# Kernel tuning notes

Measured on AMD Instinct MI355X. Metric: run time of the kernel, lower is better.

The kernel has to match this reference:

```python
import jax, jax.numpy as jnp
import numpy as np

B, T, D, H = 8, 1024, 512, 8
D4 = 4 * D
SIGMA = 16.0
EPS = 1e-5


def layer_norm(x, w, b):
    m = jnp.mean(x, axis=-1, keepdims=True)
    v = jnp.mean((x - m) ** 2, axis=-1, keepdims=True)
    return (x - m) * jax.lax.rsqrt(v + EPS) * w + b


def setup_inputs() -> dict:
    key = jax.random.key(0)
    ks = jax.random.split(key, 12)
    return {
        "x": jax.random.normal(ks[0], (B, T, D), jnp.float32),
        "posv": jax.random.randint(ks[1], (B, T), 0, 64, jnp.int32),
        "posh": jax.random.randint(ks[2], (B, T), 0, 64, jnp.int32),
        "norm1_w": jnp.ones((D,), jnp.float32),
        "norm1_b": jnp.zeros((D,), jnp.float32),
        "in_w": jax.random.normal(ks[3], (3 * D, D), jnp.float32) * (D ** -0.5),
        "in_b": jnp.zeros((3 * D,), jnp.float32),
        "out_w": jax.random.normal(ks[4], (D, D), jnp.float32) * (D ** -0.5),
        "out_b": jnp.zeros((D,), jnp.float32),
        "norm2_w": jnp.ones((D,), jnp.float32),
        "norm2_b": jnp.zeros((D,), jnp.float32),
        "w1": jax.random.normal(ks[5], (D4, D), jnp.float32) * (D ** -0.5),
        "b1": jnp.zeros((D4,), jnp.float32),
        "w2": jax.random.normal(ks[6], (D, D4), jnp.float32) * (D4 ** -0.5),
        "b2": jnp.zeros((D,), jnp.float32),
        "gate": jnp.array(0.0, jnp.float32),
    }


def reference(x, posv, posh, norm1_w, norm1_b, in_w, in_b, out_w, out_b,
              norm2_w, norm2_b, w1, b1, w2, b2, gate):
    hd = D // H
    residual = x
    xn = layer_norm(x, norm1_w, norm1_b)

    # --- standard multi-head self-attention (dropout=eval identity) ---
    qkv = xn @ in_w.T + in_b                       # [B,T,3D]
    q, k, v = jnp.split(qkv, 3, axis=-1)
    q = q.reshape(B, T, H, hd).transpose(0, 2, 1, 3)  # [B,H,T,hd]
    k = k.reshape(B, T, H, hd).transpose(0, 2, 1, 3)
    v = v.reshape(B, T, H, hd).transpose(0, 2, 1, 3)
    scores = jnp.einsum("bhqd,bhkd->bhqk", q, k) * (hd ** -0.5)
    attn = jax.nn.softmax(scores, axis=-1)
    ctx = jnp.einsum("bhqk,bhkd->bhqd", attn, v)   # [B,H,T,hd]
    ctx = ctx.transpose(0, 2, 1, 3).reshape(B, T, D)
    std_out = ctx @ out_w.T + out_b

    # --- Gaussian kernel position attention ---
    pos = jnp.stack([posv, posh], axis=-1).astype(jnp.float32)  # [B,T,2]
    dist_sq = jnp.sum((pos[:, :, None, :] - pos[:, None, :, :]) ** 2, axis=-1)  # [B,T,T]
    kw = jnp.exp(-dist_sq / (2.0 * SIGMA ** 2))
    kw = kw / jnp.sum(kw, axis=-1, keepdims=True)
    kernel_out = kw @ xn                            # [B,T,D]

    g = jax.nn.sigmoid(gate)
    x1 = residual + g * std_out + (1.0 - g) * kernel_out

    # --- MLP block ---
    xn2 = layer_norm(x1, norm2_w, norm2_b)
    h = jax.nn.gelu(xn2 @ w1.T + b1, approximate=False)
    return x1 + h @ w2.T + b2
```

## Files before the change

kernel.cpp:

```cpp
#include <hip/hip_runtime.h>
#include <hip/hip_bf16.h>
#include <math.h>

typedef unsigned short ushort_t;
typedef short short8 __attribute__((ext_vector_type(8)));
typedef float f32x4 __attribute__((ext_vector_type(4)));

__device__ __forceinline__ float b2f(ushort_t u) {
  union { unsigned u; float f; } v; v.u = ((unsigned)u) << 16; return v.f;
}
__device__ __forceinline__ ushort_t f2b(float f) {
  union { float f; unsigned u; } v; v.f = f;
  unsigned r = (v.u + 0x7FFFu + ((v.u >> 16) & 1u)) >> 16;
  return (ushort_t)r;
}
__device__ __forceinline__ float gelu_fast(float v) {
  float u = 0.7978845608f * (v + 0.044715f * v * v * v);
  float a = fabsf(u);
  float t = exp2f(a * -2.8853900817779268f);
  float th = (1.f - t) / (1.f + t);
  th = copysignf(th, u);
  return 0.5f * v * (1.f + th);
}

union U16x8 { uint4 v; ushort_t s[8]; };

typedef const __attribute__((address_space(1))) unsigned int glb_u32;
typedef __attribute__((address_space(3))) unsigned int lds_u32;
__device__ __forceinline__ void gl_lds16(const ushort_t* g, ushort_t* l) {
  __builtin_amdgcn_global_load_lds((glb_u32*)g, (lds_u32*)l, 16, 0, 0);
}

__global__ __launch_bounds__(256) void cvt4_kernel(const float* __restrict__ s0,
                                                   const float* __restrict__ s1,
                                                   const float* __restrict__ s2,
                                                   const float* __restrict__ s3,
                                                   ushort_t* __restrict__ d0,
                                                   ushort_t* __restrict__ d1,
                                                   ushort_t* __restrict__ d2,
                                                   ushort_t* __restrict__ d3) {
  long i = (long)blockIdx.x * 256 + threadIdx.x;
  const float* s; ushort_t* d; long off;
  if (i < 196608)       { s = s0; d = d0; off = i; }
  else if (i < 262144)  { s = s1; d = d1; off = i - 196608; }
  else if (i < 524288)  { s = s2; d = d2; off = i - 262144; }
  else                  { s = s3; d = d3; off = i - 524288; }
  float4 f = *(const float4*)(s + off * 4);
  union { uint2 v; ushort_t s[4]; } o;
  o.s[0] = f2b(f.x); o.s[1] = f2b(f.y); o.s[2] = f2b(f.z); o.s[3] = f2b(f.w);
  *(uint2*)(d + off * 4) = o.v;
}

__global__ __launch_bounds__(256) void ln_kernel(const float* __restrict__ x,
                                                 const float* __restrict__ w,
                                                 const float* __restrict__ b,
                                                 ushort_t* __restrict__ out) {
  int tid = threadIdx.x, wave = tid >> 6, lane = tid & 63;
  long token = (long)blockIdx.x * 4 + wave;
  const float* xr = x + token * 512 + lane * 8;
  float4 a0 = *(const float4*)xr;
  float4 a1 = *(const float4*)(xr + 4);
  float xf[8] = {a0.x, a0.y, a0.z, a0.w, a1.x, a1.y, a1.z, a1.w};
  float s = 0.f, sq = 0.f;
#pragma unroll
  for (int i = 0; i < 8; i++) { s += xf[i]; sq += xf[i] * xf[i]; }
#pragma unroll
  for (int off = 1; off < 64; off <<= 1) { s += __shfl_xor(s, off); sq += __shfl_xor(sq, off); }
  float m = s * (1.f / 512.f);
  float var = sq * (1.f / 512.f) - m * m;
  float rs = rsqrtf(var + 1e-5f);
  float4 w0 = *(const float4*)(w + lane * 8);
  float4 w1v = *(const float4*)(w + lane * 8 + 4);
  float4 b0 = *(const float4*)(b + lane * 8);
  float4 b1v = *(const float4*)(b + lane * 8 + 4);
  float wf[8] = {w0.x, w0.y, w0.z, w0.w, w1v.x, w1v.y, w1v.z, w1v.w};
  float bf[8] = {b0.x, b0.y, b0.z, b0.w, b1v.x, b1v.y, b1v.z, b1v.w};
  U16x8 o;
#pragma unroll
  for (int i = 0; i < 8; i++) o.s[i] = f2b((xf[i] - m) * rs * wf[i] + bf[i]);
  *(uint4*)(out + token * 512 + lane * 8) = o.v;
}

__global__ __launch_bounds__(256) void ln_b_kernel(const ushort_t* __restrict__ x,
                                                   const float* __restrict__ w,
                                                   const float* __restrict__ b,
                                                   ushort_t* __restrict__ out) {
  int tid = threadIdx.x, wave = tid >> 6, lane = tid & 63;
  long token = (long)blockIdx.x * 4 + wave;
  U16x8 ux; ux.v = *(const uint4*)(x + token * 512 + lane * 8);
  float xf[8], s = 0.f, sq = 0.f;
#pragma unroll
  for (int i = 0; i < 8; i++) { xf[i] = b2f(ux.s[i]); s += xf[i]; sq += xf[i] * xf[i]; }
#pragma unroll
  for (int off = 1; off < 64; off <<= 1) { s += __shfl_xor(s, off); sq += __shfl_xor(sq, off); }
  float m = s * (1.f / 512.f);
  float var = sq * (1.f / 512.f) - m * m;
  float rs = rsqrtf(var + 1e-5f);
  float4 w0 = *(const float4*)(w + lane * 8);
  float4 w1v = *(const float4*)(w + lane * 8 + 4);
  float4 b0 = *(const float4*)(b + lane * 8);
  float4 b1v = *(const float4*)(b + lane * 8 + 4);
  float wf[8] = {w0.x, w0.y, w0.z, w0.w, w1v.x, w1v.y, w1v.z, w1v.w};
  float bf[8] = {b0.x, b0.y, b0.z, b0.w, b1v.x, b1v.y, b1v.z, b1v.w};
  U16x8 o;
#pragma unroll
  for (int i = 0; i < 8; i++) o.s[i] = f2b((xf[i] - m) * rs * wf[i] + bf[i]);
  *(uint4*)(out + token * 512 + lane * 8) = o.v;
}

__global__ __launch_bounds__(256) void kw_kernel(const int* __restrict__ posv,
                                                 const int* __restrict__ posh,
                                                 ushort_t* __restrict__ kw) {
  int b = blockIdx.x >> 10, i = blockIdx.x & 1023;
  int tid = threadIdx.x;
  const int* pv = posv + b * 1024;
  const int* ph = posh + b * 1024;
  int pvi = pv[i], phi = ph[i];
  int j0 = tid * 4;
  int4 vj = *(const int4*)(pv + j0);
  int4 hj = *(const int4*)(ph + j0);
  int vv[4] = {vj.x, vj.y, vj.z, vj.w};
  int hh[4] = {hj.x, hj.y, hj.z, hj.w};
  float e[4]; float loc = 0.f;
#pragma unroll
  for (int u = 0; u < 4; u++) {
    int dv = pvi - vv[u], dh = phi - hh[u];
    e[u] = expf((float)(dv * dv + dh * dh) * (-1.f / 512.f));
    loc += e[u];
  }
#pragma unroll
  for (int off = 1; off < 64; off <<= 1) loc += __shfl_xor(loc, off);
  __shared__ float wsum[4];
  __shared__ float tot;
  if ((tid & 63) == 0) wsum[tid >> 6] = loc;
  __syncthreads();
  if (tid == 0) tot = wsum[0] + wsum[1] + wsum[2] + wsum[3];
  __syncthreads();
  float inv = 1.f / tot;
  union { uint2 v; ushort_t s[4]; } o;
#pragma unroll
  for (int u = 0; u < 4; u++) o.s[u] = f2b(e[u] * inv);
  *(uint2*)&kw[((long)(b * 1024 + i)) * 1024 + j0] = o.v;
}

__global__ __launch_bounds__(256) void tr_kernel(const ushort_t* __restrict__ in,
                                                 ushort_t* __restrict__ out,
                                                 int R, int C) {
  __shared__ ushort_t tile[64 * 64];
  int z = blockIdx.z, r0 = blockIdx.y * 64, c0 = blockIdx.x * 64;
  const ushort_t* src = in + (long)z * R * C;
  ushort_t* dst = out + (long)z * R * C;
  int tid = threadIdx.x;
  int tr = tid >> 2;
  const ushort_t* s = src + (long)(r0 + tr) * C + c0;
  int g = (tr + (tr >> 4)) & 7;
#pragma unroll
  for (int u = 0; u < 2; u++) {
    int c = (tid & 3) + u * 4;
    *(uint4*)&tile[tr * 64 + (c ^ g) * 8] = *(const uint4*)(s + c * 8);
  }
  __syncthreads();
  int oc = tid >> 2, ob = (tid & 3) * 16;
  U16x8 o0, o1;
#pragma unroll
  for (int j = 0; j < 16; j++) {
    int r = ob + j;
    int gg = (r + (r >> 4)) & 7;
    ushort_t val = tile[r * 64 + (((oc >> 3) ^ gg)) * 8 + (oc & 7)];
    if (j < 8) o0.s[j] = val; else o1.s[j - 8] = val;
  }
  ushort_t* d = dst + (long)(c0 + oc) * R + r0 + ob;
  *(uint4*)d = o0.v;
  *(uint4*)(d + 8) = o1.v;
}

struct GemmP {
  const ushort_t* A; const ushort_t* Bm;
  long sA, sB, sC;
  int lda, ldb, ldc, K;
  const float* biasf;
  const float* residf;
  const ushort_t* auxb;
  const float* auxf;
  float* outf;
  ushort_t* outb;
  ushort_t* qp; ushort_t* kp; ushort_t* vp;
  const float* gate;
};

template <int BM, int BN, int EPI>
__global__ __launch_bounds__(256) void gemm_k(GemmP p) {
  constexpr int TI = BM / 32, TJ = BN / 32;
  constexpr int RA = BM / 64, RB = BN / 64;
  __shared__ ushort_t As[2][BM * 32];
  __shared__ ushort_t Bs[2][BN * 32];
  int tid = threadIdx.x, wv = tid >> 6, lane = tid & 63;
  int quad = lane >> 4, l15 = lane & 15;
  int bl = blockIdx.x + gridDim.x * blockIdx.y;
  int m0 = (bl % gridDim.y) * BM;
  int n0 = (bl / gridDim.y) * BN;
  int z = blockIdx.z;
  const ushort_t* A = p.A + (long)z * p.sA;
  const ushort_t* Bm = p.Bm + (long)z * p.sB;
  int wm = (wv & 1) * (BM / 2), wn = (wv >> 1) * (BN / 2);
  f32x4 acc[TI][TJ];
#pragma unroll
  for (int i = 0; i < TI; i++)
#pragma unroll
    for (int j = 0; j < TJ; j++)
#pragma unroll
      for (int r = 0; r < 4; r++) acc[i][j][r] = 0.f;

  int srow = tid >> 2;
  int sc = ((tid & 3) ^ ((tid >> 3) & 3)) * 8;
  const ushort_t* ga = A + (long)(m0 + srow) * p.lda + sc;
  const ushort_t* gb = Bm + (long)(n0 + srow) * p.ldb + sc;
  long a64 = (long)64 * p.lda, b64 = (long)64 * p.ldb;
  int aswz = (quad ^ ((l15 >> 1) & 3)) * 8;
  int nsteps = p.K >> 5;

#pragma unroll
  for (int rr = 0; rr < RA; rr++)
    gl_lds16(ga + rr * a64, As[0] + rr * 2048 + wv * 512);
#pragma unroll
  for (int rr = 0; rr < RB; rr++)
    gl_lds16(gb + rr * b64, Bs[0] + rr * 2048 + wv * 512);
  __syncthreads();

  for (int ks = 0; ks < nsteps; ks++) {
    int cur = ks & 1;
    if (ks + 1 < nsteps) {
      const ushort_t* a0 = ga + (ks + 1) * 32;
      const ushort_t* b0 = gb + (ks + 1) * 32;
#pragma unroll
      for (int rr = 0; rr < RA; rr++)
        gl_lds16(a0 + rr * a64, As[cur ^ 1] + rr * 2048 + wv * 512);
#pragma unroll
      for (int rr = 0; rr < RB; rr++)
        gl_lds16(b0 + rr * b64, Bs[cur ^ 1] + rr * 2048 + wv * 512);
    }
    short8 av[TI], bv[TJ];
#pragma unroll
    for (int ti = 0; ti < TI; ti++)
      av[ti] = *(const short8*)&As[cur][(wm + ti * 16 + l15) * 32 + aswz];
#pragma unroll
    for (int tj = 0; tj < TJ; tj++)
      bv[tj] = *(const short8*)&Bs[cur][(wn + tj * 16 + l15) * 32 + aswz];
#pragma unroll
    for (int ti = 0; ti < TI; ti++)
#pragma unroll
      for (int tj = 0; tj < TJ; tj++)
        acc[ti][tj] = __builtin_amdgcn_mfma_f32_16x16x32_bf16(av[ti], bv[tj], acc[ti][tj], 0, 0, 0);
    __syncthreads();
  }

  float g = 0.f;
  if constexpr (EPI == 2) g = 1.f / (1.f + expf(-p.gate[0]));
#pragma unroll
  for (int ti = 0; ti < TI; ti++) {
#pragma unroll
    for (int tj = 0; tj < TJ; tj++) {
#pragma unroll
      for (int r = 0; r < 4; r++) {
        int gm = m0 + wm + ti * 16 + quad * 4 + r;
        int n = n0 + wn + tj * 16 + l15;
        float v = acc[ti][tj][r];
        if constexpr (EPI == 0) {
          v += p.biasf[n];
          int bb = gm >> 10, tt = gm & 1023;
          if (n < 512) {
            int h = n >> 6, d = n & 63;
            p.qp[((long)(bb * 8 + h) * 1024 + tt) * 64 + d] = f2b(v * 0.18033688011112042f);
          } else if (n < 1024) {
            int n2 = n - 512, h = n2 >> 6, d = n2 & 63;
            p.kp[((long)(bb * 8 + h) * 1024 + tt) * 64 + d] = f2b(v);
          } else {
            int n2 = n - 1024, h = n2 >> 6, d = n2 & 63;
            p.vp[((long)(bb * 8 + h) * 1024 + tt) * 64 + d] = f2b(v);
          }
        } else if constexpr (EPI == 1) {
          p.outb[(long)z * p.sC + (long)gm * p.ldc + n] = f2b(v);
        } else if constexpr (EPI == 2) {
          v += p.biasf[n];
          long idx = (long)gm * 512 + n;
          p.outb[idx] = f2b(p.residf[idx] + g * v + (1.f - g) * b2f(p.auxb[idx]));
        } else if constexpr (EPI == 3) {
          v += p.biasf[n];
          p.outb[(long)gm * p.ldc + n] = f2b(gelu_fast(v));
        } else {
          v += p.biasf[n];
          long idx = (long)gm * 512 + n;
          p.outf[idx] = v + b2f(p.auxb[idx]);
        }
      }
    }
  }
}

__global__ __launch_bounds__(256) void flash_k(const ushort_t* __restrict__ q,
                                               const ushort_t* __restrict__ k,
                                               const ushort_t* __restrict__ vT,
                                               ushort_t* __restrict__ ctx) {
  int bl = blockIdx.x + gridDim.x * blockIdx.y;
  int bh = bl % 64;
  int q0 = (bl / 64) * 128;
  int tid = threadIdx.x, wv = tid >> 6, lane = tid & 63;
  int quad = lane >> 4, l15 = lane & 15;
  __shared__ ushort_t Ks[2][64 * 64], Vt[2][64 * 64];
  __shared__ ushort_t Pt[128 * 64];
  int wm = wv * 32;

  short8 qf[2][2];
#pragma unroll
  for (int tq = 0; tq < 2; tq++)
#pragma unroll
    for (int kk = 0; kk < 2; kk++)
      qf[tq][kk] = *(const short8*)&q[((long)bh * 1024 + q0 + wm + tq * 16 + l15) * 64 + kk * 32 + quad * 8];

  int srow = tid >> 3;
  int sc = ((tid & 7) ^ ((tid >> 3) & 7)) * 8;
#pragma unroll
  for (int e = 0; e < 2; e++) {
    gl_lds16(&k[((long)bh * 1024 + e * 32 + srow) * 64 + sc], Ks[0] + e * 2048 + wv * 512);
    gl_lds16(&vT[((long)bh * 64 + e * 32 + srow) * 1024 + sc], Vt[0] + e * 2048 + wv * 512);
  }
  __syncthreads();

  f32x4 O[2][4];
#pragma unroll
  for (int tq = 0; tq < 2; tq++)
#pragma unroll
    for (int td = 0; td < 4; td++)
#pragma unroll
      for (int r = 0; r < 4; r++) O[tq][td][r] = 0.f;
  float ls[2] = {0.f, 0.f};

  int pswz = (l15 & 7) << 1;
  for (int kt = 0; kt < 16; kt++) {
    int cur = kt & 1;
    if (kt + 1 < 16) {
#pragma unroll
      for (int e = 0; e < 2; e++) {
        gl_lds16(&k[((long)bh * 1024 + (kt + 1) * 64 + e * 32 + srow) * 64 + sc], Ks[cur ^ 1] + e * 2048 + wv * 512);
        gl_lds16(&vT[((long)bh * 64 + e * 32 + srow) * 1024 + (kt + 1) * 64 + sc], Vt[cur ^ 1] + e * 2048 + wv * 512);
      }
    }
#pragma unroll
    for (int tq = 0; tq < 2; tq++) {
      f32x4 S[4];
#pragma unroll
      for (int tk = 0; tk < 4; tk++) {
#pragma unroll
        for (int r = 0; r < 4; r++) S[tk][r] = 0.f;
#pragma unroll
        for (int kk = 0; kk < 2; kk++) {
          short8 kf = *(const short8*)&Ks[cur][(tk * 16 + l15) * 64 + ((kk * 4 + quad) ^ (l15 & 7)) * 8];
          S[tk] = __builtin_amdgcn_mfma_f32_16x16x32_bf16(kf, qf[tq][kk], S[tk], 0, 0, 0);
        }
      }
#pragma unroll
      for (int tk = 0; tk < 4; tk++) {
        float p0 = exp2f(S[tk][0]);
        float p1 = exp2f(S[tk][1]);
        float p2 = exp2f(S[tk][2]);
        float p3 = exp2f(S[tk][3]);
        ls[tq] += (p0 + p1) + (p2 + p3);
        unsigned lo = __builtin_amdgcn_perm(__float_as_uint(p1), __float_as_uint(p0), 0x07060302u);
        unsigned hi = __builtin_amdgcn_perm(__float_as_uint(p3), __float_as_uint(p2), 0x07060302u);
        int gnum = (tk * 4 + quad) ^ pswz;
        uint2 pr; pr.x = lo; pr.y = hi;
        *(uint2*)&Pt[(wm + tq * 16 + l15) * 64 + gnum * 4] = pr;
      }
    }
#pragma unroll
    for (int tq = 0; tq < 2; tq++) {
#pragma unroll
      for (int kk = 0; kk < 2; kk++) {
        short8 pf = *(const short8*)&Pt[(wm + tq * 16 + l15) * 64 + (((kk * 8 + quad * 2) ^ pswz)) * 4];
#pragma unroll
        for (int td = 0; td < 4; td++) {
          short8 vf = *(const short8*)&Vt[cur][(td * 16 + l15) * 64 + ((kk * 4 + quad) ^ (l15 & 7)) * 8];
          O[tq][td] = __builtin_amdgcn_mfma_f32_16x16x32_bf16(pf, vf, O[tq][td], 0, 0, 0);
        }
      }
    }
    __syncthreads();
  }
#pragma unroll
  for (int tq = 0; tq < 2; tq++) {
    ls[tq] += __shfl_xor(ls[tq], 16);
    ls[tq] += __shfl_xor(ls[tq], 32);
  }
  int bb = bh >> 3, h = bh & 7;
#pragma unroll
  for (int tq = 0; tq < 2; tq++) {
#pragma unroll
    for (int r = 0; r < 4; r++) {
      int qrow = quad * 4 + r;
      float inv = 1.f / __shfl(ls[tq], (lane & 48) | qrow);
      long row = (long)bb * 1024 + q0 + wm + tq * 16 + qrow;
#pragma unroll
      for (int td = 0; td < 4; td++)
        ctx[row * 512 + h * 64 + td * 16 + l15] = f2b(O[tq][td][r] * inv);
    }
  }
}

extern "C" void kernel_launch(void* const* d_in, const int* in_sizes, int n_in,
                              void* d_out, int out_size, void* d_ws, size_t ws_size,
                              hipStream_t stream) {
  const float* x    = (const float*)d_in[0];
  const int* posv   = (const int*)d_in[1];
  const int* posh   = (const int*)d_in[2];
  const float* n1w  = (const float*)d_in[3];
  const float* n1b  = (const float*)d_in[4];
  const float* in_w = (const float*)d_in[5];
  const float* in_b = (const float*)d_in[6];
  const float* outw = (const float*)d_in[7];
  const float* outb = (const float*)d_in[8];
  const float* n2w  = (const float*)d_in[9];
  const float* n2b  = (const float*)d_in[10];
  const float* w1   = (const float*)d_in[11];
  const float* b1   = (const float*)d_in[12];
  const float* w2   = (const float*)d_in[13];
  const float* b2   = (const float*)d_in[14];
  const float* gate = (const float*)d_in[15];
  float* out = (float*)d_out;

  char* ws = (char*)d_ws;
  const size_t MB = 1024 * 1024;
  ushort_t* q    = (ushort_t*)(ws + 0 * MB);
  ushort_t* kk   = (ushort_t*)(ws + 8 * MB);
  ushort_t* vtmp = (ushort_t*)(ws + 16 * MB);
  ushort_t* vT   = (ushort_t*)(ws + 24 * MB);
  ushort_t* kw   = (ushort_t*)(ws + 32 * MB);
  ushort_t* xn   = (ushort_t*)(ws + 48 * MB);
  ushort_t* xnT  = (ushort_t*)(ws + 56 * MB);
  ushort_t* ctx  = (ushort_t*)(ws + 64 * MB);
  ushort_t* ko   = (ushort_t*)(ws + 72 * MB);
  ushort_t* x1b  = (ushort_t*)(ws + 80 * MB);
  ushort_t* xn2  = (ushort_t*)(ws + 16 * MB);
  ushort_t* inwb = (ushort_t*)(ws + 96 * MB);
  ushort_t* owb  = (ushort_t*)(ws + 98 * MB);
  ushort_t* w1b  = (ushort_t*)(ws + 99 * MB);
  ushort_t* w2b  = (ushort_t*)(ws + 101 * MB);
  ushort_t* h    = (ushort_t*)(ws + 24 * MB);

  cvt4_kernel<<<3072, 256, 0, stream>>>(in_w, outw, w1, w2, inwb, owb, w1b, w2b);
  ln_kernel<<<2048, 256, 0, stream>>>(x, n1w, n1b, xn);
  kw_kernel<<<8192, 256, 0, stream>>>(posv, posh, kw);
  {
    GemmP p = {};
    p.A = xn; p.Bm = inwb; p.lda = 512; p.ldb = 512; p.K = 512;
    p.biasf = in_b; p.qp = q; p.kp = kk; p.vp = vtmp;
    gemm_k<128, 128, 0><<<dim3(12, 64, 1), 256, 0, stream>>>(p);
  }
  tr_kernel<<<dim3(1, 16, 64), 256, 0, stream>>>(vtmp, vT, 1024, 64);
  flash_k<<<dim3(8, 64, 1), 256, 0, stream>>>(q, kk, vT, ctx);
  tr_kernel<<<dim3(8, 16, 8), 256, 0, stream>>>(xn, xnT, 1024, 512);
  {
    GemmP p = {};
    p.A = kw; p.Bm = xnT; p.lda = 1024; p.ldb = 1024; p.ldc = 512; p.K = 1024;
    p.sA = 1024L * 1024; p.sB = 512L * 1024; p.sC = 1024L * 512;
    p.outb = ko;
    gemm_k<64, 128, 1><<<dim3(4, 16, 8), 256, 0, stream>>>(p);
  }
  {
    GemmP p = {};
    p.A = ctx; p.Bm = owb; p.lda = 512; p.ldb = 512; p.K = 512;
    p.biasf = outb; p.residf = x; p.auxb = ko; p.outb = x1b; p.gate = gate;
    gemm_k<64, 64, 2><<<dim3(8, 128, 1), 256, 0, stream>>>(p);
  }
  ln_b_kernel<<<2048, 256, 0, stream>>>(x1b, n2w, n2b, xn2);
  {
    GemmP p = {};
    p.A = xn2; p.Bm = w1b; p.lda = 512; p.ldb = 512; p.ldc = 2048; p.K = 512;
    p.biasf = b1; p.outb = h;
    gemm_k<128, 128, 3><<<dim3(16, 64, 1), 256, 0, stream>>>(p);
  }
  {
    GemmP p = {};
    p.A = h; p.Bm = w2b; p.lda = 2048; p.ldb = 2048; p.K = 2048;
    p.biasf = b2; p.auxb = x1b; p.outf = out;
    gemm_k<64, 128, 4><<<dim3(4, 128, 1), 256, 0, stream>>>(p);
  }
}
```

Measured before the change: 296.1 us.

## Add 256x256-tile 8-wave GEMM kernel for QKV and MLP-up projections

After: 298.7 us. No clear change (+0.9%).

```diff
diff --git a/kernel.cpp b/kernel.cpp
--- a/kernel.cpp
+++ b/kernel.cpp
@@ -297,6 +297,172 @@
   }
 }
 
+template <int EPI>
+__global__ __launch_bounds__(512, 2) void gemm256_k(GemmP p) {
+  __shared__ __align__(16) ushort_t As[2][256 * 64];
+  __shared__ __align__(16) ushort_t Bs[2][256 * 64];
+  int tid = threadIdx.x, wv = tid >> 6, lane = tid & 63;
+  int quad = lane >> 4, l15 = lane & 15;
+  int m0 = blockIdx.x * 256, n0 = blockIdx.y * 256;
+  int wr = wv >> 2, wc = wv & 3;
+
+  int srow = tid >> 3;
+  int scol = ((tid & 7) ^ (srow & 7)) * 8;
+  const ushort_t* ga = p.A + (long)(m0 + srow) * p.lda + scol;
+  const ushort_t* gb = p.Bm + (long)(n0 + srow) * p.ldb + scol;
+  long a64 = (long)64 * p.lda, b64 = (long)64 * p.ldb;
+  int NT = p.K >> 6;
+
+  f32x4 acc[8][4];
+#pragma unroll
+  for (int i = 0; i < 8; i++)
+#pragma unroll
+    for (int j = 0; j < 4; j++)
+#pragma unroll
+      for (int r = 0; r < 4; r++) acc[i][j][r] = 0.f;
+
+  gl_lds16(gb + 0 * b64, Bs[0] + 0 * 4096 + wv * 512);
+  gl_lds16(gb + 1 * b64, Bs[0] + 1 * 4096 + wv * 512);
+  gl_lds16(gb + 2 * b64, Bs[0] + 2 * 4096 + wv * 512);
+  gl_lds16(gb + 3 * b64, Bs[0] + 3 * 4096 + wv * 512);
+  gl_lds16(ga + 0 * a64, As[0] + 0 * 4096 + wv * 512);
+  gl_lds16(ga + 2 * a64, As[0] + 2 * 4096 + wv * 512);
+  gl_lds16(ga + 1 * a64, As[0] + 1 * 4096 + wv * 512);
+  gl_lds16(ga + 3 * a64, As[0] + 3 * 4096 + wv * 512);
+  asm volatile("s_waitcnt vmcnt(2)" ::: "memory");
+  __builtin_amdgcn_s_barrier();
+
+  int c0 = (quad ^ (l15 & 7)) * 8;
+  int c1 = ((quad + 4) ^ (l15 & 7)) * 8;
+
+  for (int t = 0; t < NT; t++) {
+    int bt = t & 1, nx = bt ^ 1;
+    bool pre = (t + 1 < NT);
+    const ushort_t* Ab = &As[bt][(wr * 128 + l15) * 64];
+    const ushort_t* Bb = &Bs[bt][(wc * 64 + l15) * 64];
+    const ushort_t* gak = ga + (t + 1) * 64;
+    const ushort_t* gbk = gb + (t + 1) * 64;
+    short8 a[8], bn0[4], bn1[4];
+
+#pragma unroll
+    for (int mf = 0; mf < 4; mf++) {
+      a[2 * mf]     = *(const short8*)(Ab + mf * 1024 + c0);
+      a[2 * mf + 1] = *(const short8*)(Ab + mf * 1024 + c1);
+    }
+#pragma unroll
+    for (int nf = 0; nf < 2; nf++) {
+      bn0[2 * nf]     = *(const short8*)(Bb + nf * 1024 + c0);
+      bn0[2 * nf + 1] = *(const short8*)(Bb + nf * 1024 + c1);
+    }
+    if (pre) {
+      gl_lds16(gbk + 0 * b64, Bs[nx] + 0 * 4096 + wv * 512);
+      gl_lds16(gbk + 1 * b64, Bs[nx] + 1 * 4096 + wv * 512);
+    }
+    __builtin_amdgcn_s_barrier();
+    __builtin_amdgcn_s_setprio(1);
+#pragma unroll
+    for (int mf = 0; mf < 4; mf++)
+#pragma unroll
+      for (int nf = 0; nf < 2; nf++) {
+        acc[mf][nf] = __builtin_amdgcn_mfma_f32_16x16x32_bf16(a[2 * mf], bn0[2 * nf], acc[mf][nf], 0, 0, 0);
+        acc[mf][nf] = __builtin_amdgcn_mfma_f32_16x16x32_bf16(a[2 * mf + 1], bn0[2 * nf + 1], acc[mf][nf], 0, 0, 0);
+      }
+    __builtin_amdgcn_s_setprio(0);
+    __builtin_amdgcn_s_barrier();
+
+#pragma unroll
+    for (int nf = 0; nf < 2; nf++) {
+      bn1[2 * nf]     = *(const short8*)(Bb + (2 + nf) * 1024 + c0);
+      bn1[2 * nf + 1] = *(const short8*)(Bb + (2 + nf) * 1024 + c1);
+    }
+    if (pre) {
+      gl_lds16(gbk + 2 * b64, Bs[nx] + 2 * 4096 + wv * 512);
+      gl_lds16(gbk + 3 * b64, Bs[nx] + 3 * 4096 + wv * 512);
+    }
+    __builtin_amdgcn_s_barrier();
+    __builtin_amdgcn_s_setprio(1);
+#pragma unroll
+    for (int mf = 0; mf < 4; mf++)
+#pragma unroll
+      for (int nf = 0; nf < 2; nf++) {
+        acc[mf][2 + nf] = __builtin_amdgcn_mfma_f32_16x16x32_bf16(a[2 * mf], bn1[2 * nf], acc[mf][2 + nf], 0, 0, 0);
+        acc[mf][2 + nf] = __builtin_amdgcn_mfma_f32_16x16x32_bf16(a[2 * mf + 1], bn1[2 * nf + 1], acc[mf][2 + nf], 0, 0, 0);
+      }
+    __builtin_amdgcn_s_setprio(0);
+    if (pre) asm volatile("s_waitcnt vmcnt(4)" ::: "memory");
+    else     asm volatile("s_waitcnt vmcnt(0)" ::: "memory");
+    __builtin_amdgcn_s_barrier();
+
+#pragma unroll
+    for (int mf = 0; mf < 4; mf++) {
+      a[2 * mf]     = *(const short8*)(Ab + (4 + mf) * 1024 + c0);
+      a[2 * mf + 1] = *(const short8*)(Ab + (4 + mf) * 1024 + c1);
+    }
+    if (pre) {
+      gl_lds16(gak + 0 * a64, As[nx] + 0 * 4096 + wv * 512);
+      gl_lds16(gak + 2 * a64, As[nx] + 2 * 4096 + wv * 512);
+    }
+    __builtin_amdgcn_s_barrier();
+    __builtin_amdgcn_s_setprio(1);
+#pragma unroll
+    for (int mf = 0; mf < 4; mf++)
+#pragma unroll
+      for (int nf = 0; nf < 2; nf++) {
+        acc[4 + mf][2 + nf] = __builtin_amdgcn_mfma_f32_16x16x32_bf16(a[2 * mf], bn1[2 * nf], acc[4 + mf][2 + nf], 0, 0, 0);
+        acc[4 + mf][2 + nf] = __builtin_amdgcn_mfma_f32_16x16x32_bf16(a[2 * mf + 1], bn1[2 * nf + 1], acc[4 + mf][2 + nf], 0, 0, 0);
+      }
+    __builtin_amdgcn_s_setprio(0);
+    __builtin_amdgcn_s_barrier();
+
+    if (pre) {
+      gl_lds16(gak + 1 * a64, As[nx] + 1 * 4096 + wv * 512);
+      gl_lds16(gak + 3 * a64, As[nx] + 3 * 4096 + wv * 512);
+    }
+    __builtin_amdgcn_s_barrier();
+    __builtin_amdgcn_s_setprio(1);
+#pragma unroll
+    for (int mf = 0; mf < 4; mf++)
+#pragma unroll
+      for (int nf = 0; nf < 2; nf++) {
+        acc[4 + mf][nf] = __builtin_amdgcn_mfma_f32_16x16x32_bf16(a[2 * mf], bn0[2 * nf], acc[4 + mf][nf], 0, 0, 0);
+        acc[4 + mf][nf] = __builtin_amdgcn_mfma_f32_16x16x32_bf16(a[2 * mf + 1], bn0[2 * nf + 1], acc[4 + mf][nf], 0, 0, 0);
+      }
+    __builtin_amdgcn_s_setprio(0);
+    if (pre) asm volatile("s_waitcnt vmcnt(2)" ::: "memory");
+    __builtin_amdgcn_s_barrier();
+  }
+
+#pragma unroll
+  for (int mf = 0; mf < 8; mf++) {
+#pragma unroll
+    for (int nf = 0; nf < 4; nf++) {
+#pragma unroll
+      for (int r = 0; r < 4; r++) {
+        int gm = m0 + wr * 128 + mf * 16 + quad * 4 + r;
+        int n = n0 + wc * 64 + nf * 16 + l15;
+        float v = acc[mf][nf][r];
+        if constexpr (EPI == 0) {
+          v += p.biasf[n];
+          int bb = gm >> 10, tt = gm & 1023;
+          if (n < 512) {
+            int h = n >> 6, d = n & 63;
+            p.qp[((long)(bb * 8 + h) * 1024 + tt) * 64 + d] = f2b(v * 0.18033688011112042f);
+          } else if (n < 1024) {
+            int n2 = n - 512, h = n2 >> 6, d = n2 & 63;
+            p.kp[((long)(bb * 8 + h) * 1024 + tt) * 64 + d] = f2b(v);
+          } else {
+            int n2 = n - 1024, h = n2 >> 6, d = n2 & 63;
+            p.vp[((long)(bb * 8 + h) * 1024 + tt) * 64 + d] = f2b(v);
+          }
+        } else {
+          v += p.biasf[n];
+          p.outb[(long)gm * p.ldc + n] = f2b(gelu_fast(v));
+        }
+      }
+    }
+  }
+}
+
 __global__ __launch_bounds__(256) void flash_k(const ushort_t* __restrict__ q,
                                                const ushort_t* __restrict__ k,
                                                const ushort_t* __restrict__ vT,
@@ -453,7 +619,7 @@
     GemmP p = {};
     p.A = xn; p.Bm = inwb; p.lda = 512; p.ldb = 512; p.K = 512;
     p.biasf = in_b; p.qp = q; p.kp = kk; p.vp = vtmp;
-    gemm_k<128, 128, 0><<<dim3(12, 64, 1), 256, 0, stream>>>(p);
+    gemm256_k<0><<<dim3(32, 6), 512, 0, stream>>>(p);
   }
   tr_kernel<<<dim3(1, 16, 64), 256, 0, stream>>>(vtmp, vT, 1024, 64);
   flash_k<<<dim3(8, 64, 1), 256, 0, stream>>>(q, kk, vT, ctx);
@@ -476,7 +642,7 @@
     GemmP p = {};
     p.A = xn2; p.Bm = w1b; p.lda = 512; p.ldb = 512; p.ldc = 2048; p.K = 512;
     p.biasf = b1; p.outb = h;
-    gemm_k<128, 128, 3><<<dim3(16, 64, 1), 256, 0, stream>>>(p);
+    gemm256_k<3><<<dim3(32, 8), 512, 0, stream>>>(p);
   }
   {
     GemmP p = {};
```

## Use 4-stage LDS pipeline in GEMM, drop barriers in flash, shrink tiles

Applied to the files above, without the earlier changes.

Result: faster. 288.2 us (-2.6%).

```diff
diff --git a/kernel.cpp b/kernel.cpp
--- a/kernel.cpp
+++ b/kernel.cpp
@@ -192,8 +192,8 @@
 __global__ __launch_bounds__(256) void gemm_k(GemmP p) {
   constexpr int TI = BM / 32, TJ = BN / 32;
   constexpr int RA = BM / 64, RB = BN / 64;
-  __shared__ ushort_t As[2][BM * 32];
-  __shared__ ushort_t Bs[2][BN * 32];
+  __shared__ ushort_t As[4][BM * 32];
+  __shared__ ushort_t Bs[4][BN * 32];
   int tid = threadIdx.x, wv = tid >> 6, lane = tid & 63;
   int quad = lane >> 4, l15 = lane & 15;
   int bl = blockIdx.x + gridDim.x * blockIdx.y;
@@ -220,38 +220,48 @@
   int nsteps = p.K >> 5;
 
 #pragma unroll
-  for (int rr = 0; rr < RA; rr++)
-    gl_lds16(ga + rr * a64, As[0] + rr * 2048 + wv * 512);
-#pragma unroll
-  for (int rr = 0; rr < RB; rr++)
-    gl_lds16(gb + rr * b64, Bs[0] + rr * 2048 + wv * 512);
-  __syncthreads();
-
-  for (int ks = 0; ks < nsteps; ks++) {
-    int cur = ks & 1;
-    if (ks + 1 < nsteps) {
-      const ushort_t* a0 = ga + (ks + 1) * 32;
-      const ushort_t* b0 = gb + (ks + 1) * 32;
-#pragma unroll
-      for (int rr = 0; rr < RA; rr++)
-        gl_lds16(a0 + rr * a64, As[cur ^ 1] + rr * 2048 + wv * 512);
-#pragma unroll
-      for (int rr = 0; rr < RB; rr++)
-        gl_lds16(b0 + rr * b64, Bs[cur ^ 1] + rr * 2048 + wv * 512);
-    }
-    short8 av[TI], bv[TJ];
-#pragma unroll
-    for (int ti = 0; ti < TI; ti++)
-      av[ti] = *(const short8*)&As[cur][(wm + ti * 16 + l15) * 32 + aswz];
-#pragma unroll
-    for (int tj = 0; tj < TJ; tj++)
-      bv[tj] = *(const short8*)&Bs[cur][(wn + tj * 16 + l15) * 32 + aswz];
-#pragma unroll
-    for (int ti = 0; ti < TI; ti++)
+  for (int s = 0; s < 2; s++) {
+#pragma unroll
+    for (int rr = 0; rr < RA; rr++)
+      gl_lds16(ga + s * 32 + rr * a64, As[s] + rr * 2048 + wv * 512);
+#pragma unroll
+    for (int rr = 0; rr < RB; rr++)
+      gl_lds16(gb + s * 32 + rr * b64, Bs[s] + rr * 2048 + wv * 512);
+  }
+
+  for (int ks = 0; ks < nsteps; ks += 2) {
+    asm volatile("s_waitcnt vmcnt(0)" ::: "memory");
+    __builtin_amdgcn_s_barrier();
+    if (ks + 2 < nsteps) {
+#pragma unroll
+      for (int s = 0; s < 2; s++) {
+        int st = ks + 2 + s, bf = st & 3;
+        const ushort_t* a0 = ga + st * 32;
+        const ushort_t* b0 = gb + st * 32;
+#pragma unroll
+        for (int rr = 0; rr < RA; rr++)
+          gl_lds16(a0 + rr * a64, As[bf] + rr * 2048 + wv * 512);
+#pragma unroll
+        for (int rr = 0; rr < RB; rr++)
+          gl_lds16(b0 + rr * b64, Bs[bf] + rr * 2048 + wv * 512);
+      }
+    }
+#pragma unroll
+    for (int hs = 0; hs < 2; hs++) {
+      int cur = (ks + hs) & 3;
+      short8 av[TI], bv[TJ];
+#pragma unroll
+      for (int ti = 0; ti < TI; ti++)
+        av[ti] = *(const short8*)&As[cur][(wm + ti * 16 + l15) * 32 + aswz];
 #pragma unroll
       for (int tj = 0; tj < TJ; tj++)
-        acc[ti][tj] = __builtin_amdgcn_mfma_f32_16x16x32_bf16(av[ti], bv[tj], acc[ti][tj], 0, 0, 0);
-    __syncthreads();
+        bv[tj] = *(const short8*)&Bs[cur][(wn + tj * 16 + l15) * 32 + aswz];
+#pragma unroll
+      for (int ti = 0; ti < TI; ti++)
+#pragma unroll
+        for (int tj = 0; tj < TJ; tj++)
+          acc[ti][tj] = __builtin_amdgcn_mfma_f32_16x16x32_bf16(av[ti], bv[tj], acc[ti][tj], 0, 0, 0);
+    }
   }
 
   float g = 0.f;
@@ -324,7 +334,6 @@
     gl_lds16(&k[((long)bh * 1024 + e * 32 + srow) * 64 + sc], Ks[0] + e * 2048 + wv * 512);
     gl_lds16(&vT[((long)bh * 64 + e * 32 + srow) * 1024 + sc], Vt[0] + e * 2048 + wv * 512);
   }
-  __syncthreads();
 
   f32x4 O[2][4];
 #pragma unroll
@@ -338,6 +347,8 @@
   int pswz = (l15 & 7) << 1;
   for (int kt = 0; kt < 16; kt++) {
     int cur = kt & 1;
+    asm volatile("s_waitcnt vmcnt(0)" ::: "memory");
+    __builtin_amdgcn_s_barrier();
     if (kt + 1 < 16) {
 #pragma unroll
       for (int e = 0; e < 2; e++) {
@@ -384,7 +395,6 @@
         }
       }
     }
-    __syncthreads();
   }
 #pragma unroll
   for (int tq = 0; tq < 2; tq++) {
@@ -453,7 +463,7 @@
     GemmP p = {};
     p.A = xn; p.Bm = inwb; p.lda = 512; p.ldb = 512; p.K = 512;
     p.biasf = in_b; p.qp = q; p.kp = kk; p.vp = vtmp;
-    gemm_k<128, 128, 0><<<dim3(12, 64, 1), 256, 0, stream>>>(p);
+    gemm_k<64, 128, 0><<<dim3(12, 128, 1), 256, 0, stream>>>(p);
   }
   tr_kernel<<<dim3(1, 16, 64), 256, 0, stream>>>(vtmp, vT, 1024, 64);
   flash_k<<<dim3(8, 64, 1), 256, 0, stream>>>(q, kk, vT, ctx);
@@ -476,7 +486,7 @@
     GemmP p = {};
     p.A = xn2; p.Bm = w1b; p.lda = 512; p.ldb = 512; p.ldc = 2048; p.K = 512;
     p.biasf = b1; p.outb = h;
-    gemm_k<128, 128, 3><<<dim3(16, 64, 1), 256, 0, stream>>>(p);
+    gemm_k<64, 128, 3><<<dim3(16, 128, 1), 256, 0, stream>>>(p);
   }
   {
     GemmP p = {};
```
